# Kernel optimization log

Measured on AMD Instinct MI355X. Metric: run time of the kernel, lower is better.

## Reference

```python
import jax, jax.numpy as jnp
import numpy as np

B, T_OUT, C, L = 8, 8, 64, 1024  # batch, temporal channels, spatial channels (=in_channels), time steps


def setup_inputs() -> dict:
    key = jax.random.key(0)
    ks = jax.random.split(key, 7)
    s = 1.0 / np.sqrt(C)  # conv1d default init scale
    return {
        "x": jax.random.normal(ks[0], (B, T_OUT, C, L), dtype=jnp.float32),
        "Wq": jax.random.uniform(ks[1], (C, C), jnp.float32, -s, s),
        "bq": jax.random.uniform(ks[2], (C,), jnp.float32, -s, s),
        "Wk": jax.random.uniform(ks[3], (C, C), jnp.float32, -s, s),
        "bk": jax.random.uniform(ks[4], (C,), jnp.float32, -s, s),
        "Wv": jax.random.uniform(ks[5], (C, C), jnp.float32, -s, s),
        "bv": jax.random.uniform(ks[6], (C,), jnp.float32, -s, s),
    }


def reference(x, Wq, bq, Wk, bk, Wv, bv):
    b, t, c, l = x.shape
    xr = x.reshape(b * t, c, l)  # [BT, C, L]
    # 1x1 Conv1d == per-timestep linear over channels
    q = jnp.einsum('oc,bcl->bol', Wq, xr) + bq[:, None]
    k = jnp.einsum('oc,bcl->bol', Wk, xr) + bk[:, None]
    v = jnp.einsum('oc,bcl->bol', Wv, xr) + bv[:, None]
    # scores[b, i, j] = sum_c q[b, c, i] * k[b, c, j]  -> [BT, L, L]
    scores = jnp.einsum('bci,bcj->bij', q, k)
    weights = jax.nn.softmax(scores, axis=-1)
    # out[b, i, c] = sum_j weights[b, i, j] * v[b, c, j]
    out = jnp.einsum('bij,bcj->bic', weights, v)
    out = jnp.transpose(out, (0, 2, 1))  # [BT, C, L]
    return out.reshape(b, t, c, l)
```

## Files before the change

### kernel.cpp

```cpp
#include <hip/hip_runtime.h>
#include <hip/hip_bf16.h>

#define CC 64
#define LL 1024
#define LOG2E 1.44269504f

typedef unsigned short u16;
typedef unsigned int u32;
typedef __attribute__((ext_vector_type(8))) short short8;
typedef __attribute__((ext_vector_type(4))) float floatx4;

static __device__ __forceinline__ u16 f2b(float f) {
  return (u16)((__float_as_uint(f) + 0x8000u) >> 16);
}
static __device__ __forceinline__ u32 pk2(float a, float b) {
  return ((__float_as_uint(a) + 0x8000u) >> 16) |
         ((__float_as_uint(b) + 0x8000u) & 0xffff0000u);
}
static __device__ __forceinline__ u32 pk2t(float a, float b) {
  return __builtin_amdgcn_perm(__float_as_uint(b), __float_as_uint(a), 0x07060302u);
}

__global__ __launch_bounds__(256) void w_prep(
    const float* __restrict__ Wq, const float* __restrict__ bq,
    const float* __restrict__ Wk, const float* __restrict__ bk,
    const float* __restrict__ Wv, const float* __restrict__ bv,
    u16* __restrict__ whi, float* __restrict__ bsc)
{
  const int idx = blockIdx.x * 256 + threadIdx.x;
  const int m = idx >> 12;
  const float* W = (m == 0) ? Wq : (m == 1) ? Wk : Wv;
  const float w = W[idx & 4095] * ((m == 0) ? LOG2E : 1.0f);
  whi[idx] = f2b(w);
  if (blockIdx.x == 0 && threadIdx.x < 192)
    bsc[threadIdx.x] = (threadIdx.x < 64) ? bq[threadIdx.x] * LOG2E
                     : (threadIdx.x < 128) ? bk[threadIdx.x - 64] : bv[threadIdx.x - 128];
}

__global__ __launch_bounds__(256) void qkv_kernel(
    const float* __restrict__ x,
    const u16* __restrict__ whi, const float* __restrict__ bsc,
    u16* __restrict__ qT, u16* __restrict__ kT, u16* __restrict__ vO)
{
  __shared__ __align__(16) u16 xh_s[2][64 * 72];
  __shared__ __align__(16) u16 tbuf[4 * 16 * 72];
  __shared__ float b_s[192];

  const int tid  = threadIdx.x;
  const int wave = tid >> 6;
  const int lane = tid & 63;
  const int l16  = lane & 15;
  const int quad = lane >> 4;

  const int bt = blockIdx.x & 63;
  const int l0 = (blockIdx.x >> 6) << 7;

  const int lx = tid & 63;
  const int cg = (tid >> 6) << 4;
  const float* xp = x + ((size_t)bt * CC + cg) * LL + l0 + lx;

  {
    float v0[16];
    #pragma unroll
    for (int e = 0; e < 16; ++e) v0[e] = xp[(size_t)e * LL];
    #pragma unroll
    for (int e = 0; e < 16; e += 2)
      *(u32*)(&xh_s[0][0] + lx * 72 + cg + e) = pk2(v0[e], v0[e + 1]);
    if (tid < 192) b_s[tid] = bsc[tid];
  }
  __syncthreads();

  float v1[16];
  #pragma unroll
  for (int e = 0; e < 16; ++e) v1[e] = xp[64 + (size_t)e * LL];

  u16* tb = tbuf + wave * (16 * 72);

  auto compute = [&](int ch) {
    const int lc0 = l0 + (ch << 6);
    const u16* xr_h = &xh_s[ch][0] + (wave * 16 + l16) * 72 + quad * 8;
    const short8 xh0 = *(const short8*)(xr_h);
    const short8 xh1 = *(const short8*)(xr_h + 32);

    #pragma unroll
    for (int ot = 0; ot < 12; ++ot) {
      const int m = ot >> 2;
      const int off = (m << 12) + (((ot & 3) * 16 + l16) << 6) + quad * 8;
      const short8 ah0 = *(const short8*)(whi + off);
      const short8 ah1 = *(const short8*)(whi + off + 32);

      floatx4 acc = (floatx4){0.f, 0.f, 0.f, 0.f};
      acc = __builtin_amdgcn_mfma_f32_16x16x32_bf16(ah0, xh0, acc, 0, 0, 0);
      acc = __builtin_amdgcn_mfma_f32_16x16x32_bf16(ah1, xh1, acc, 0, 0, 0);

      float ov[4];
      #pragma unroll
      for (int r = 0; r < 4; ++r)
        ov[r] = acc[r] + b_s[ot * 16 + quad * 4 + r];

      if (ot < 8) {
        uint2 pv;
        pv.x = pk2(ov[0], ov[1]);
        pv.y = pk2(ov[2], ov[3]);
        *(uint2*)(tb + l16 * 72 + (ot & 3) * 16 + quad * 4) = pv;
        if ((ot & 3) == 3) {
          asm volatile("" ::: "memory");
          u16* gdst = ((ot < 4) ? qT : kT) + ((size_t)(bt * LL + lc0 + wave * 16)) * CC;
          const int rr = lane >> 3;
          const int c8 = (lane & 7) * 8;
          #pragma unroll
          for (int s2 = 0; s2 < 2; ++s2) {
            const int row = s2 * 8 + rr;
            uint4 val = *(const uint4*)(tb + row * 72 + c8);
            *(uint4*)(gdst + row * CC + c8) = val;
          }
          asm volatile("" ::: "memory");
        }
      } else {
        const int ob = (ot - 8) * 16 + quad * 4;
        u16* vdst = vO + ((size_t)(bt * CC + ob)) * LL + lc0 + wave * 16 + l16;
        #pragma unroll
        for (int r = 0; r < 4; ++r)
          vdst[(size_t)r * LL] = f2b(ov[r]);
      }
    }
  };

  compute(0);

  #pragma unroll
  for (int e = 0; e < 16; e += 2)
    *(u32*)(&xh_s[1][0] + lx * 72 + cg + e) = pk2(v1[e], v1[e + 1]);
  __syncthreads();

  compute(1);
}

__global__ __launch_bounds__(256) void attn_kernel(
    const u16* __restrict__ qT, const u16* __restrict__ kT,
    const u16* __restrict__ vB, float* __restrict__ out)
{
  __shared__ __align__(16) u16 smem[23040];
  u16* p_s = smem + 18432;

  const int tid  = threadIdx.x;
  const int wave = tid >> 6;
  const int lane = tid & 63;
  const int l16  = lane & 15;
  const int quad = lane >> 4;

  const int bt    = blockIdx.x & 63;
  const int chunk = blockIdx.x >> 6;
  const int i0w   = (chunk << 7) + (wave << 5);

  const u16* kbase = kT + (size_t)bt * LL * CC;
  const u16* vbase = vB + (size_t)bt * CC * LL;

  short8 qf[2][2];
  {
    const u16* qb = qT + (size_t)bt * LL * CC;
    #pragma unroll
    for (int s = 0; s < 2; ++s) {
      const u16* qr = qb + (size_t)(i0w + s * 16 + l16) * CC + quad * 8;
      qf[s][0] = *(const short8*)(qr);
      qf[s][1] = *(const short8*)(qr + 32);
    }
  }

  floatx4 O[2][4];
  #pragma unroll
  for (int s = 0; s < 2; ++s)
    #pragma unroll
    for (int cf = 0; cf < 4; ++cf)
      O[s][cf] = (floatx4){0.f, 0.f, 0.f, 0.f};
  float lsA[2] = {0.f, 0.f}, lsB[2] = {0.f, 0.f};

  const int r_st = tid >> 2;
  const int c_st = (tid & 3) << 4;
  u16* pw = p_s + wave * (16 * 72);

  {
    uint4 k0 = *(const uint4*)(kbase + (size_t)r_st * CC + c_st);
    uint4 k1 = *(const uint4*)(kbase + (size_t)r_st * CC + c_st + 8);
    uint4 v0 = *(const uint4*)(vbase + (size_t)r_st * LL + c_st);
    uint4 v1 = *(const uint4*)(vbase + (size_t)r_st * LL + c_st + 8);
    *(uint4*)(smem + r_st * 72 + c_st)            = k0;
    *(uint4*)(smem + r_st * 72 + c_st + 8)        = k1;
    *(uint4*)(smem + 4608 + r_st * 72 + c_st)     = v0;
    *(uint4*)(smem + 4608 + r_st * 72 + c_st + 8) = v1;
  }
  __syncthreads();

  for (int it = 0; it < 16; ++it) {
    u16* ktc = smem + (it & 1) * 9216;
    u16* vtc = ktc + 4608;

    uint4 rk0, rk1, rv0, rv1;
    if (it < 15) {
      const int jb = (it + 1) << 6;
      rk0 = *(const uint4*)(kbase + (size_t)(jb + r_st) * CC + c_st);
      rk1 = *(const uint4*)(kbase + (size_t)(jb + r_st) * CC + c_st + 8);
      rv0 = *(const uint4*)(vbase + (size_t)r_st * LL + jb + c_st);
      rv1 = *(const uint4*)(vbase + (size_t)r_st * LL + jb + c_st + 8);
    }

    floatx4 S[2][4];
    #pragma unroll
    for (int jt = 0; jt < 4; ++jt) {
      const u16* ka = ktc + (jt * 16 + l16) * 72 + quad * 8;
      const short8 a0 = *(const short8*)(ka);
      const short8 a1 = *(const short8*)(ka + 32);
      #pragma unroll
      for (int s = 0; s < 2; ++s) {
        floatx4 acc = (floatx4){0.f, 0.f, 0.f, 0.f};
        acc = __builtin_amdgcn_mfma_f32_16x16x32_bf16(a0, qf[s][0], acc, 0, 0, 0);
        acc = __builtin_amdgcn_mfma_f32_16x16x32_bf16(a1, qf[s][1], acc, 0, 0, 0);
        S[s][jt] = acc;
      }
    }

    short8 v0f[4], v1f[4];
    #pragma unroll
    for (int cf = 0; cf < 4; ++cf) {
      const u16* va = vtc + (cf * 16 + l16) * 72 + quad * 8;
      v0f[cf] = *(const short8*)(va);
      v1f[cf] = *(const short8*)(va + 32);
    }

    #pragma unroll
    for (int s = 0; s < 2; ++s) {
      u16* pwr = pw + l16 * 72 + quad * 4;
      #pragma unroll
      for (int jt = 0; jt < 4; ++jt) {
        const float e0 = __builtin_amdgcn_exp2f(S[s][jt][0]);
        const float e1 = __builtin_amdgcn_exp2f(S[s][jt][1]);
        const float e2 = __builtin_amdgcn_exp2f(S[s][jt][2]);
        const float e3 = __builtin_amdgcn_exp2f(S[s][jt][3]);
        lsA[s] += e0 + e1;
        lsB[s] += e2 + e3;
        uint2 pv;
        pv.x = pk2t(e0, e1);
        pv.y = pk2t(e2, e3);
        *(uint2*)(pwr + jt * 16) = pv;
      }
      asm volatile("" ::: "memory");

      const u16* pr = pw + l16 * 72 + quad * 8;
      const short8 p0 = *(const short8*)(pr);
      const short8 p1 = *(const short8*)(pr + 32);
      #pragma unroll
      for (int cf = 0; cf < 4; ++cf) {
        O[s][cf] = __builtin_amdgcn_mfma_f32_16x16x32_bf16(p0, v0f[cf], O[s][cf], 0, 0, 0);
        O[s][cf] = __builtin_amdgcn_mfma_f32_16x16x32_bf16(p1, v1f[cf], O[s][cf], 0, 0, 0);
      }
      asm volatile("" ::: "memory");
    }

    if (it < 15) {
      u16* ktn = smem + ((it + 1) & 1) * 9216;
      *(uint4*)(ktn + r_st * 72 + c_st)            = rk0;
      *(uint4*)(ktn + r_st * 72 + c_st + 8)        = rk1;
      *(uint4*)(ktn + 4608 + r_st * 72 + c_st)     = rv0;
      *(uint4*)(ktn + 4608 + r_st * 72 + c_st + 8) = rv1;
    }
    __syncthreads();
  }

  float lsum[2];
  #pragma unroll
  for (int s = 0; s < 2; ++s) {
    lsum[s] = lsA[s] + lsB[s];
    lsum[s] += __shfl_xor(lsum[s], 16, 64);
    lsum[s] += __shfl_xor(lsum[s], 32, 64);
  }

  __syncthreads();
  float* of = (float*)smem + wave * 1280;
  #pragma unroll
  for (int s = 0; s < 2; ++s) {
    #pragma unroll
    for (int r = 0; r < 4; ++r) {
      const float rl = __builtin_amdgcn_rcpf(__shfl(lsum[s], quad * 4 + r, 64));
      #pragma unroll
      for (int cf = 0; cf < 4; ++cf)
        O[s][cf][r] *= rl;
    }
    asm volatile("" ::: "memory");
    #pragma unroll
    for (int cf = 0; cf < 4; ++cf)
      #pragma unroll
      for (int r = 0; r < 4; ++r)
        of[(cf * 16 + l16) * 20 + quad * 4 + r] = O[s][cf][r];
    asm volatile("" ::: "memory");
    float* ob = out + ((size_t)bt * CC) * LL + i0w + s * 16;
    #pragma unroll
    for (int rr = 0; rr < 4; ++rr) {
      const int c = rr * 16 + l16;
      float4 val = *(const float4*)(of + c * 20 + quad * 4);
      *(float4*)(ob + (size_t)c * LL + quad * 4) = val;
    }
    asm volatile("" ::: "memory");
  }
}

extern "C" void kernel_launch(void* const* d_in, const int* in_sizes, int n_in,
                              void* d_out, int out_size, void* d_ws, size_t ws_size,
                              hipStream_t stream) {
  const float* x  = (const float*)d_in[0];
  const float* Wq = (const float*)d_in[1];
  const float* bq = (const float*)d_in[2];
  const float* Wk = (const float*)d_in[3];
  const float* bk = (const float*)d_in[4];
  const float* Wv = (const float*)d_in[5];
  const float* bv = (const float*)d_in[6];
  float* out = (float*)d_out;

  u16* qTp = (u16*)d_ws;
  u16* kTp = qTp + (size_t)64 * LL * CC;
  u16* vp  = kTp + (size_t)64 * LL * CC;
  u16* whi = vp  + (size_t)64 * LL * CC;
  float* bsc = (float*)(whi + 3 * 64 * 64);

  w_prep<<<48, 256, 0, stream>>>(Wq, bq, Wk, bk, Wv, bv, whi, bsc);
  qkv_kernel<<<512, 256, 0, stream>>>(x, whi, bsc, qTp, kTp, vp);
  attn_kernel<<<512, 256, 0, stream>>>(qTp, kTp, vp, out);
}
```

Measured before the change: 120.9 us.

## Keep softmax probabilities in registers by permuting K rows in shared memory

K rows are stored into shared memory under a permuted row index, so the S=K·Q MFMA output lanes already match the A-operand layout needed by the P·V MFMA. The exponentiated probabilities are packed straight into short8 register fragments instead of going through a per-wave LDS scratch buffer. This removes LDS writes and reads plus a serialization point per tile, and shrinks shared memory use. It relies on the row permutation exactly matching the MFMA lane mapping, which is easy to get subtly wrong.

```diff
diff --git a/kernel.cpp b/kernel.cpp
--- a/kernel.cpp
+++ b/kernel.cpp
@@ -19,6 +19,11 @@
 }
 static __device__ __forceinline__ u32 pk2t(float a, float b) {
   return __builtin_amdgcn_perm(__float_as_uint(b), __float_as_uint(a), 0x07060302u);
+}
+static __device__ __forceinline__ short8 mk8(u32 a, u32 b, u32 c, u32 d) {
+  union { u32 u[4]; short8 s; } t;
+  t.u[0] = a; t.u[1] = b; t.u[2] = c; t.u[3] = d;
+  return t.s;
 }
 
 __global__ __launch_bounds__(256) void w_prep(
@@ -140,9 +145,7 @@
     const u16* __restrict__ qT, const u16* __restrict__ kT,
     const u16* __restrict__ vB, float* __restrict__ out)
 {
-  __shared__ __align__(16) u16 smem[23040];
-  u16* p_s = smem + 18432;
-
+  __shared__ __align__(16) u16 smem[18432];
   const int tid  = threadIdx.x;
   const int wave = tid >> 6;
   const int lane = tid & 63;
@@ -177,15 +180,15 @@
 
   const int r_st = tid >> 2;
   const int c_st = (tid & 3) << 4;
-  u16* pw = p_s + wave * (16 * 72);
+  const int sr = (r_st & 0x20) | ((r_st & 4) << 2) | ((r_st & 0x18) >> 1) | (r_st & 3);
 
   {
     uint4 k0 = *(const uint4*)(kbase + (size_t)r_st * CC + c_st);
     uint4 k1 = *(const uint4*)(kbase + (size_t)r_st * CC + c_st + 8);
     uint4 v0 = *(const uint4*)(vbase + (size_t)r_st * LL + c_st);
     uint4 v1 = *(const uint4*)(vbase + (size_t)r_st * LL + c_st + 8);
-    *(uint4*)(smem + r_st * 72 + c_st)            = k0;
-    *(uint4*)(smem + r_st * 72 + c_st + 8)        = k1;
+    *(uint4*)(smem + sr * 72 + c_st)              = k0;
+    *(uint4*)(smem + sr * 72 + c_st + 8)          = k1;
     *(uint4*)(smem + 4608 + r_st * 72 + c_st)     = v0;
     *(uint4*)(smem + 4608 + r_st * 72 + c_st + 8) = v1;
   }
@@ -219,17 +222,9 @@
       }
     }
 
-    short8 v0f[4], v1f[4];
-    #pragma unroll
-    for (int cf = 0; cf < 4; ++cf) {
-      const u16* va = vtc + (cf * 16 + l16) * 72 + quad * 8;
-      v0f[cf] = *(const short8*)(va);
-      v1f[cf] = *(const short8*)(va + 32);
-    }
-
-    #pragma unroll
-    for (int s = 0; s < 2; ++s) {
-      u16* pwr = pw + l16 * 72 + quad * 4;
+    uint2 pp[2][4];
+    #pragma unroll
+    for (int s = 0; s < 2; ++s)
       #pragma unroll
       for (int jt = 0; jt < 4; ++jt) {
         const float e0 = __builtin_amdgcn_exp2f(S[s][jt][0]);
@@ -238,28 +233,33 @@
         const float e3 = __builtin_amdgcn_exp2f(S[s][jt][3]);
         lsA[s] += e0 + e1;
         lsB[s] += e2 + e3;
-        uint2 pv;
-        pv.x = pk2t(e0, e1);
-        pv.y = pk2t(e2, e3);
-        *(uint2*)(pwr + jt * 16) = pv;
+        pp[s][jt].x = pk2t(e0, e1);
+        pp[s][jt].y = pk2t(e2, e3);
       }
-      asm volatile("" ::: "memory");
-
-      const u16* pr = pw + l16 * 72 + quad * 8;
-      const short8 p0 = *(const short8*)(pr);
-      const short8 p1 = *(const short8*)(pr + 32);
+
+    short8 v0f[4], v1f[4];
+    #pragma unroll
+    for (int cf = 0; cf < 4; ++cf) {
+      const u16* va = vtc + (cf * 16 + l16) * 72 + quad * 8;
+      v0f[cf] = *(const short8*)(va);
+      v1f[cf] = *(const short8*)(va + 32);
+    }
+
+    #pragma unroll
+    for (int s = 0; s < 2; ++s) {
+      const short8 pa0 = mk8(pp[s][0].x, pp[s][0].y, pp[s][1].x, pp[s][1].y);
+      const short8 pa1 = mk8(pp[s][2].x, pp[s][2].y, pp[s][3].x, pp[s][3].y);
       #pragma unroll
       for (int cf = 0; cf < 4; ++cf) {
-        O[s][cf] = __builtin_amdgcn_mfma_f32_16x16x32_bf16(p0, v0f[cf], O[s][cf], 0, 0, 0);
-        O[s][cf] = __builtin_amdgcn_mfma_f32_16x16x32_bf16(p1, v1f[cf], O[s][cf], 0, 0, 0);
+        O[s][cf] = __builtin_amdgcn_mfma_f32_16x16x32_bf16(pa0, v0f[cf], O[s][cf], 0, 0, 0);
+        O[s][cf] = __builtin_amdgcn_mfma_f32_16x16x32_bf16(pa1, v1f[cf], O[s][cf], 0, 0, 0);
       }
-      asm volatile("" ::: "memory");
     }
 
     if (it < 15) {
       u16* ktn = smem + ((it + 1) & 1) * 9216;
-      *(uint4*)(ktn + r_st * 72 + c_st)            = rk0;
-      *(uint4*)(ktn + r_st * 72 + c_st + 8)        = rk1;
+      *(uint4*)(ktn + sr * 72 + c_st)              = rk0;
+      *(uint4*)(ktn + sr * 72 + c_st + 8)          = rk1;
       *(uint4*)(ktn + 4608 + r_st * 72 + c_st)     = rv0;
       *(uint4*)(ktn + 4608 + r_st * 72 + c_st + 8) = rv1;
     }
```

Result: no change. 118.8 us (-1.7%).
